# Performance work log

Hardware: AMD Instinct MI355X
Metric: run time of the kernel (lower is better)

The kernel has to match this reference:

```python
import jax, jax.numpy as jnp
import numpy as np

N = 30000      # nodes
E = 480000     # edges
F = 128        # num_node_features (== C, required by LSTM-JK stacking of h_list incl. x)
C = 128        # graph_hidden_channels
K = 8          # kernel_size (num gaussians)
D = 2          # pseudo-coordinate dim
L = 4          # nlayers
H = (L * C) // 2   # PyG JK-LSTM hidden size = 256
NHID = 512
NOUT = 256
B = 1024       # number of graphs in batch
EPS = 1e-15


def setup_inputs() -> dict:
    key = jax.random.key(0)
    ks = jax.random.split(key, 24)
    s = 0.05
    inp = {}
    inp['x'] = jax.random.normal(ks[0], (N, F), jnp.float32)
    inp['edge_index'] = jax.random.randint(ks[1], (2, E), 0, N, dtype=jnp.int32)
    inp['edge_attr'] = jax.random.uniform(ks[2], (E, D), jnp.float32)
    inp['batch'] = jnp.sort(jax.random.randint(ks[3], (N,), 0, B, dtype=jnp.int32))
    # GMMConv params per layer (Cin == C for all layers since F == C)
    inp['g'] = jax.random.normal(ks[4], (L, F, K * C), jnp.float32) * s
    inp['root'] = jax.random.normal(ks[5], (L, F, C), jnp.float32) * s
    inp['bias'] = jnp.zeros((L, C), jnp.float32)
    inp['mu'] = jax.random.uniform(ks[6], (L, K, D), jnp.float32)
    inp['sigma'] = jax.random.uniform(ks[7], (L, K, D), jnp.float32) * 0.5 + 0.5
    inp['bn_gamma'] = jnp.ones((L, C), jnp.float32)
    inp['bn_beta'] = jnp.zeros((L, C), jnp.float32)
    # Bidirectional LSTM for JumpingKnowledge: dir 0 = fwd, dir 1 = bwd; gate order i,f,g,o
    inp['w_ih'] = jax.random.normal(ks[8], (2, 4 * H, C), jnp.float32) * s
    inp['w_hh'] = jax.random.normal(ks[9], (2, 4 * H, H), jnp.float32) * s
    inp['b_ih'] = jnp.zeros((2, 4 * H), jnp.float32)
    inp['b_hh'] = jnp.zeros((2, 4 * H), jnp.float32)
    inp['att_w'] = jax.random.normal(ks[10], (2 * H, 1), jnp.float32) * s
    inp['att_b'] = jnp.zeros((1,), jnp.float32)
    inp['p1_w'] = jax.random.normal(ks[11], (C, NHID), jnp.float32) * s
    inp['p1_b'] = jnp.zeros((NHID,), jnp.float32)
    inp['p2_w'] = jax.random.normal(ks[12], (NHID, NOUT), jnp.float32) * s
    inp['p2_b'] = jnp.zeros((NOUT,), jnp.float32)
    inp['ln_g'] = jnp.ones((NOUT,), jnp.float32)
    inp['ln_b'] = jnp.zeros((NOUT,), jnp.float32)
    return inp


def _lstm_dir(xs, w_ih, w_hh, b_ih, b_hh, reverse):
    # xs: [T, N, C] -> hidden states [T, N, H], aligned with input order
    def step(carry, xt):
        h, c = carry
        gates = xt @ w_ih.T + h @ w_hh.T + (b_ih + b_hh)
        i, f, g, o = jnp.split(gates, 4, axis=-1)
        c = jax.nn.sigmoid(f) * c + jax.nn.sigmoid(i) * jnp.tanh(g)
        h = jax.nn.sigmoid(o) * jnp.tanh(c)
        return (h, c), h
    h0 = jnp.zeros((xs.shape[1], w_hh.shape[1]), xs.dtype)
    _, hs = jax.lax.scan(step, (h0, h0), xs, reverse=reverse)
    return hs


def reference(x, edge_index, edge_attr, batch, g, root, bias, mu, sigma,
              bn_gamma, bn_beta, w_ih, w_hh, b_ih, b_hh, att_w, att_b,
              p1_w, p1_b, p2_w, p2_b, ln_g, ln_b):
    src, dst = edge_index[0], edge_index[1]
    deg = jnp.maximum(jax.ops.segment_sum(jnp.ones((E,), x.dtype), dst, num_segments=N), 1.0)[:, None]
    h = x
    h_list = [x]
    for i in range(L):
        # GMMConv: node-level transform then gaussian-weighted message passing (mean aggr)
        xg = (h @ g[i]).reshape(N, K, C)                     # [N, K, C]
        diff = edge_attr[:, None, :] - mu[i][None]           # [E, K, D]
        w = jnp.exp(jnp.sum(-0.5 * diff ** 2 / (EPS + sigma[i][None] ** 2), axis=-1))  # [E, K]
        msg = jnp.zeros((E, C), x.dtype)
        for k in range(K):                                   # small fixed K; avoids [E,K,C] gather
            msg = msg + w[:, k:k + 1] * xg[src, k, :]
        agg = jax.ops.segment_sum(msg, dst, num_segments=N) / deg
        h = agg + h @ root[i] + bias[i]
        # BatchNorm1d (training-mode batch statistics)
        mean = h.mean(0)
        var = h.var(0)
        h = (h - mean) / jnp.sqrt(var + 1e-5) * bn_gamma[i] + bn_beta[i]
        if i < L - 1:
            h = jax.nn.relu(h)
        # dropout is identity in eval mode
        h_list.append(h)
    # JumpingKnowledge, mode='lstm'
    xs = jnp.stack(h_list, axis=0)                           # [L+1, N, C]
    hf = _lstm_dir(xs, w_ih[0], w_hh[0], b_ih[0], b_hh[0], False)
    hb = _lstm_dir(xs, w_ih[1], w_hh[1], b_ih[1], b_hh[1], True)
    seq = jnp.concatenate([hf, hb], axis=-1)                 # [L+1, N, 2H]
    alpha = (seq @ att_w)[..., 0] + att_b[0]                 # [L+1, N]
    alpha = jax.nn.softmax(alpha, axis=0)
    node_rep = jnp.sum(alpha[..., None] * xs, axis=0)        # [N, C]
    # global_mean_pool
    cnt = jnp.maximum(jax.ops.segment_sum(jnp.ones((N,), x.dtype), batch, num_segments=B), 1.0)
    h_graph = jax.ops.segment_sum(node_rep, batch, num_segments=B) / cnt[:, None]
    z = jax.nn.relu(h_graph @ p1_w + p1_b)
    z = z @ p2_w + p2_b
    zm = z.mean(-1, keepdims=True)
    zv = z.var(-1, keepdims=True)
    return (z - zm) / jnp.sqrt(zv + 1e-5) * ln_g + ln_b
```

## Files before the change

kernel.cpp:

```cpp
#include <hip/hip_runtime.h>
#include <hip/hip_bf16.h>
#include <math.h>

#define N_    30000
#define E_    480000
#define C_    128
#define K_    8
#define L_    4
#define H_    256
#define NHID_ 512
#define NOUT_ 256
#define B_    1024
#define SCAN_B 30

typedef __attribute__((ext_vector_type(8))) short short8;
typedef __attribute__((ext_vector_type(4))) float floatx4;
typedef __hip_bfloat16 bf16;

static inline size_t align256(size_t x){ return (x + 255) & ~(size_t)255; }

__device__ __forceinline__ void gload_lds16(const void* g, void* l){
  __builtin_amdgcn_global_load_lds((const __attribute__((address_space(1))) void*)g,
                                   (__attribute__((address_space(3))) void*)l, 16, 0, 0);
}
__device__ __forceinline__ float sigm_f(float x){ return __builtin_amdgcn_rcpf(1.f + __expf(-x)); }
__device__ __forceinline__ float tanh_f(float x){ return 1.f - 2.f*__builtin_amdgcn_rcpf(1.f + __expf(2.f*x)); }

__global__ void hist_k(const int* __restrict__ dst, int* __restrict__ cnt){
  int e = blockIdx.x*256 + threadIdx.x;
  if (e < E_) atomicAdd(&cnt[dst[e]], 1);
}

__global__ void scan1_k(const int* __restrict__ cnt, int* __restrict__ rowptr, int* __restrict__ btot){
  __shared__ int sh[1024];
  int i = blockIdx.x*1024 + (int)threadIdx.x;
  int v = (i < N_) ? cnt[i] : 0;
  sh[threadIdx.x] = v;
  __syncthreads();
  for (int o = 1; o < 1024; o <<= 1){
    int t = (threadIdx.x >= (unsigned)o) ? sh[threadIdx.x - o] : 0;
    __syncthreads();
    sh[threadIdx.x] += t;
    __syncthreads();
  }
  if (i < N_) rowptr[i] = sh[threadIdx.x] - v;
  if (threadIdx.x == 1023) btot[blockIdx.x] = sh[1023];
}
__global__ void scan2_k(const int* __restrict__ btot, int* __restrict__ boff){
  if (threadIdx.x == 0){
    int s = 0;
    for (int b = 0; b < SCAN_B; b++){ boff[b] = s; s += btot[b]; }
    boff[SCAN_B] = s;
  }
}
__global__ void scan3_k(int* __restrict__ rowptr, const int* __restrict__ boff){
  int i = blockIdx.x*1024 + (int)threadIdx.x;
  if (i < N_) rowptr[i] += boff[blockIdx.x];
  if (i == N_-1) rowptr[N_] = boff[SCAN_B];
}

__global__ void degf_k(const int* __restrict__ cnt, float* __restrict__ degf){
  int n = blockIdx.x*256 + threadIdx.x;
  if (n < N_) degf[n] = fmaxf((float)cnt[n], 1.0f);
}

__global__ void scatter_k(const int* __restrict__ src, const int* __restrict__ dst,
                          const int* __restrict__ rowptr, int* __restrict__ fill,
                          int* __restrict__ srcsort, int* __restrict__ edgepos){
  int e = blockIdx.x*256 + threadIdx.x;
  if (e >= E_) return;
  int d = dst[e];
  int pos = rowptr[d] + atomicAdd(&fill[d], 1);
  srcsort[pos] = src[e];
  edgepos[e] = pos;
}

__global__ void cast_k(const float* __restrict__ in, bf16* __restrict__ out, int n){
  int i = blockIdx.x*256 + threadIdx.x;
  if (i < n) out[i] = __float2bfloat16(in[i]);
}
__global__ void tcast_k(const float* __restrict__ in, bf16* __restrict__ out, int R, int Cc){
  const float* ip = in + (size_t)blockIdx.y*R*Cc;
  bf16* op = out + (size_t)blockIdx.y*R*Cc;
  int i = blockIdx.x*256 + threadIdx.x;
  if (i >= R*Cc) return;
  int c = i / R, r = i - c*R;
  op[i] = __float2bfloat16(ip[(size_t)r*Cc + c]);
}
__global__ void gtcast_k(const float* __restrict__ in, bf16* __restrict__ out){
  const float* ip = in + (size_t)blockIdx.y*C_*(K_*C_);
  bf16* op = out + (size_t)blockIdx.y*C_*(K_*C_);
  int i = blockIdx.x*256 + threadIdx.x;
  int co = i >> 10;
  int rem = i & 1023;
  int k = rem >> 7, c = rem & 127;
  op[i] = __float2bfloat16(ip[(size_t)c*(K_*C_) + k*C_ + co]);
}
__global__ void permcast_k(const float* __restrict__ in, bf16* __restrict__ out, int Kdim){
  const float* ip = in + (size_t)blockIdx.y*1024*Kdim;
  bf16* op = out + (size_t)blockIdx.y*1024*Kdim;
  int i = blockIdx.x*256 + threadIdx.x;
  if (i >= 1024*Kdim) return;
  int r = i / Kdim, k = i - r*Kdim;
  int gsel = r >> 8, jj = r & 255;
  int p = ((jj >> 5) << 7) + (((jj >> 4) & 1) << 6) + (gsel << 4) + (jj & 15);
  op[(size_t)p*Kdim + k] = __float2bfloat16(ip[i]);
}
__global__ void biassum_k(const float* __restrict__ bih, const float* __restrict__ bhh,
                          float* __restrict__ bs){
  int i = blockIdx.x*256 + threadIdx.x;
  if (i < 2048) bs[i] = bih[i] + bhh[i];
}

template<int OUTBF16, int STATS>
__global__ __launch_bounds__(256)
void gemm_bf16_k(const bf16* __restrict__ A1, const bf16* __restrict__ B1, int K1,
                 const bf16* __restrict__ A2, const bf16* __restrict__ B2, int K2,
                 const float* __restrict__ bias1, const float* __restrict__ bias2,
                 void* __restrict__ Cout, int M, int Nn, int relu,
                 float* __restrict__ stats)
{
  __shared__ short As[128*32];
  __shared__ short Bs[128*32];
  __shared__ float colstat[256];
  const int tid  = threadIdx.x;
  const int wave = tid >> 6, lane = tid & 63;
  const int m0 = blockIdx.y*128, n0 = blockIdx.x*128;
  const int wm = (wave >> 1)*64, wn = (wave & 1)*64;
  const int lrow = lane & 15, lk = lane >> 4;
  floatx4 acc[4][4] = {};
  if (STATS) colstat[tid] = 0.f;

  #pragma unroll
  for (int phase = 0; phase < 2; ++phase){
    const bf16* A = phase ? A2 : A1;
    const bf16* B = phase ? B2 : B1;
    const int   K = phase ? K2 : K1;
    if (A == nullptr) continue;
    for (int k0 = 0; k0 < K; k0 += 32){
      #pragma unroll
      for (int i = 0; i < 2; ++i){
        const int chunkbase = i*256 + wave*64;
        const int c   = chunkbase + lane;
        const int row = c >> 2, cc = (c & 3) << 3;
        int ar = m0 + row; if (ar >= M) ar = M - 1;
        gload_lds16(A + (size_t)ar*K + k0 + cc,        As + (size_t)chunkbase*8);
        gload_lds16(B + (size_t)(n0 + row)*K + k0 + cc, Bs + (size_t)chunkbase*8);
      }
      __syncthreads();
      short8 af[4], bfr[4];
      #pragma unroll
      for (int t = 0; t < 4; ++t){
        af[t]  = *(const short8*)&As[((size_t)(wm + t*16 + lrow))*32 + lk*8];
        bfr[t] = *(const short8*)&Bs[((size_t)(wn + t*16 + lrow))*32 + lk*8];
      }
      #pragma unroll
      for (int mt = 0; mt < 4; ++mt)
        #pragma unroll
        for (int nt = 0; nt < 4; ++nt)
          acc[mt][nt] = __builtin_amdgcn_mfma_f32_16x16x32_bf16(af[mt], bfr[nt], acc[mt][nt], 0, 0, 0);
      __syncthreads();
    }
  }

  float* outf = (float*)Cout;
  bf16*  outb = (bf16*)Cout;
  #pragma unroll
  for (int nt = 0; nt < 4; ++nt){
    const int col = n0 + wn + nt*16 + lrow;
    float bv = bias1 ? bias1[col] : 0.f;
    if (bias2) bv += bias2[col];
    float s = 0.f, s2 = 0.f;
    #pragma unroll
    for (int mt = 0; mt < 4; ++mt){
      #pragma unroll
      for (int r = 0; r < 4; ++r){
        const int row = m0 + wm + mt*16 + lk*4 + r;
        if (row >= M) continue;
        float v = acc[mt][nt][r] + bv;
        if (relu) v = fmaxf(v, 0.f);
        if (OUTBF16) outb[(size_t)row*Nn + col] = __float2bfloat16(v);
        else         outf[(size_t)row*Nn + col] = v;
        if (STATS){ s += v; s2 += v*v; }
      }
    }
    if (STATS){
      s  += __shfl_down(s, 16);  s  += __shfl_down(s, 32);
      s2 += __shfl_down(s2, 16); s2 += __shfl_down(s2, 32);
      if (lane < 16){
        atomicAdd(&colstat[wn + nt*16 + lane], s);
        atomicAdd(&colstat[128 + wn + nt*16 + lane], s2);
      }
    }
  }
  if (STATS){
    __syncthreads();
    if (tid < 128){
      atomicAdd(&stats[tid],       colstat[tid]);
      atomicAdd(&stats[128 + tid], colstat[128 + tid]);
    }
  }
}

__global__ __launch_bounds__(256)
void lstm_step_k(const bf16* __restrict__ A1, const bf16* __restrict__ B1,
                 const bf16* __restrict__ A2, const bf16* __restrict__ B2,
                 const float* __restrict__ bsum,
                 bf16* __restrict__ hout, bf16* __restrict__ cst,
                 const float* __restrict__ attw, float* __restrict__ alpha,
                 int M)
{
  __shared__ short As[128*32];
  __shared__ short Bs[128*32];
  const int tid  = threadIdx.x;
  const int wave = tid >> 6, lane = tid & 63;
  const int m0 = blockIdx.y*128, n0 = blockIdx.x*128;
  const int wm = (wave >> 1)*64, wn = (wave & 1)*64;
  const int lrow = lane & 15, lk = lane >> 4;
  floatx4 acc[4][4] = {};

  #pragma unroll
  for (int phase = 0; phase < 2; ++phase){
    const bf16* A = phase ? A2 : A1;
    const bf16* B = phase ? B2 : B1;
    const int   K = phase ? H_ : C_;
    if (A == nullptr) continue;
    for (int k0 = 0; k0 < K; k0 += 32){
      #pragma unroll
      for (int i = 0; i < 2; ++i){
        const int chunkbase = i*256 + wave*64;
        const int c   = chunkbase + lane;
        const int row = c >> 2, cc = (c & 3) << 3;
        int ar = m0 + row; if (ar >= M) ar = M - 1;
        gload_lds16(A + (size_t)ar*K + k0 + cc,        As + (size_t)chunkbase*8);
        gload_lds16(B + (size_t)(n0 + row)*K + k0 + cc, Bs + (size_t)chunkbase*8);
      }
      __syncthreads();
      short8 af[4], bfr[4];
      #pragma unroll
      for (int t = 0; t < 4; ++t){
        af[t]  = *(const short8*)&As[((size_t)(wm + t*16 + lrow))*32 + lk*8];
        bfr[t] = *(const short8*)&Bs[((size_t)(wn + t*16 + lrow))*32 + lk*8];
      }
      #pragma unroll
      for (int mt = 0; mt < 4; ++mt)
        #pragma unroll
        for (int nt = 0; nt < 4; ++nt)
          acc[mt][nt] = __builtin_amdgcn_mfma_f32_16x16x32_bf16(af[mt], bfr[nt], acc[mt][nt], 0, 0, 0);
      __syncthreads();
    }
  }

  const int j  = blockIdx.x*32 + (wave & 1)*16 + lrow;
  const float bi = bsum[0*H_ + j], bff = bsum[1*H_ + j];
  const float bg = bsum[2*H_ + j], bo  = bsum[3*H_ + j];
  const float aw = attw[j];
  #pragma unroll
  for (int mt = 0; mt < 4; ++mt){
    #pragma unroll
    for (int r = 0; r < 4; ++r){
      const int row = m0 + wm + mt*16 + lk*4 + r;
      const bool ok = row < M;
      const size_t idx = (size_t)row*H_ + j;
      float co = 0.f;
      if (A2 && ok) co = __bfloat162float(cst[idx]);
      float ig = sigm_f(acc[mt][0][r] + bi);
      float fg = sigm_f(acc[mt][1][r] + bff);
      float gt = tanh_f(acc[mt][2][r] + bg);
      float og = sigm_f(acc[mt][3][r] + bo);
      float cv = fg*co + ig*gt;
      float hv = og*tanh_f(cv);
      if (ok){
        cst[idx]  = __float2bfloat16(cv);
        hout[idx] = __float2bfloat16(hv);
      }
      float att = ok ? hv*aw : 0.f;
      att += __shfl_xor(att, 1);
      att += __shfl_xor(att, 2);
      att += __shfl_xor(att, 4);
      att += __shfl_xor(att, 8);
      if (lrow == 0 && ok) atomicAdd(&alpha[row], att);
    }
  }
}

__global__ void compute_w_k(const float* __restrict__ ea, const float* __restrict__ mu,
                            const float* __restrict__ sigma, const int* __restrict__ edgepos,
                            float* __restrict__ wsrt)
{
  int e = blockIdx.x*256 + threadIdx.x;
  if (e >= E_) return;
  float a0 = ea[2*e], a1 = ea[2*e+1];
  int pos = edgepos[e];
  float outv[8];
  #pragma unroll
  for (int k = 0; k < 8; k++){
    float d0 = a0 - mu[2*k],   d1 = a1 - mu[2*k+1];
    float s0 = sigma[2*k],     s1 = sigma[2*k+1];
    float t = -0.5f*(d0*d0/(1e-15f + s0*s0) + d1*d1/(1e-15f + s1*s1));
    outv[k] = expf(t);
  }
  float4* op = (float4*)(wsrt + (size_t)pos*8);
  op[0] = make_float4(outv[0], outv[1], outv[2], outv[3]);
  op[1] = make_float4(outv[4], outv[5], outv[6], outv[7]);
}

__global__ __launch_bounds__(256)
void aggregate_t_k(const bf16* __restrict__ h, const float* __restrict__ wsrt,
                   const int* __restrict__ rowptr, const int* __restrict__ srcsort,
                   const float* __restrict__ degf, bf16* __restrict__ t)
{
  int node = blockIdx.x*4 + (threadIdx.x >> 6);
  int lane = threadIdx.x & 63;
  if (node >= N_) return;
  int p0 = rowptr[node], p1 = rowptr[node+1];
  float ax[8] = {}, ay[8] = {};
  for (int p = p0; p < p1; p++){
    int s = srcsort[p];
    const float4 w03 = *(const float4*)(wsrt + (size_t)p*8);
    const float4 w47 = *(const float4*)(wsrt + (size_t)p*8 + 4);
    const float wk[8] = {w03.x,w03.y,w03.z,w03.w,w47.x,w47.y,w47.z,w47.w};
    float2 v = __bfloat1622float2(((const __hip_bfloat162*)(h + (size_t)s*C_))[lane]);
    #pragma unroll
    for (int k = 0; k < 8; k++){
      ax[k] = fmaf(wk[k], v.x, ax[k]);
      ay[k] = fmaf(wk[k], v.y, ay[k]);
    }
  }
  float inv = 1.0f / degf[node];
  __hip_bfloat162* tp = (__hip_bfloat162*)(t + (size_t)node*(K_*C_));
  #pragma unroll
  for (int k = 0; k < 8; k++){
    __hip_bfloat162 o; o.x = __float2bfloat16(ax[k]*inv); o.y = __float2bfloat16(ay[k]*inv);
    tp[k*64 + lane] = o;
  }
}

__global__ void bn_apply_k(const float* __restrict__ hpre, const float* __restrict__ stats,
                           const float* __restrict__ gamma, const float* __restrict__ beta,
                           bf16* __restrict__ outp, int relu)
{
  int i = blockIdx.x*256 + threadIdx.x;
  if (i >= N_*C_) return;
  int c = i & 127;
  float mean = stats[c] * (1.0f/N_);
  float var  = stats[c+128] * (1.0f/N_) - mean*mean;
  float rstd = rsqrtf(var + 1e-5f);
  float v = (hpre[i] - mean)*rstd*gamma[c] + beta[c];
  if (relu) v = fmaxf(v, 0.f);
  outp[i] = __float2bfloat16(v);
}

__global__ void jk_pool_k(const float* __restrict__ x, const bf16* __restrict__ hlist,
                          const float* __restrict__ alpha, const int* __restrict__ batch,
                          float* __restrict__ hgraph, float* __restrict__ gcnt)
{
  int n = blockIdx.x, c = threadIdx.x;
  float a[5]; float mx = -1e30f;
  #pragma unroll
  for (int t = 0; t < 5; t++){ a[t] = alpha[(size_t)t*N_ + n]; mx = fmaxf(mx, a[t]); }
  float ssum = 0.f;
  #pragma unroll
  for (int t = 0; t < 5; t++){ a[t] = expf(a[t] - mx); ssum += a[t]; }
  float inv = 1.0f/ssum;
  float val = a[0]*inv*x[(size_t)n*C_ + c];
  #pragma unroll
  for (int t = 1; t < 5; t++)
    val = fmaf(a[t]*inv, __bfloat162float(hlist[((size_t)(t-1)*N_ + n)*C_ + c]), val);
  int bg = batch[n];
  atomicAdd(&hgraph[(size_t)bg*C_ + c], val);
  if (c == 0) atomicAdd(&gcnt[bg], 1.0f);
}

__global__ void pool_div_k(const float* __restrict__ hg, const float* __restrict__ gcnt,
                           bf16* __restrict__ hgb){
  int i = blockIdx.x*256 + threadIdx.x;
  if (i < B_*C_) hgb[i] = __float2bfloat16(hg[i] / fmaxf(gcnt[i >> 7], 1.0f));
}

__global__ __launch_bounds__(256)
void layernorm_k(float* __restrict__ z, const float* __restrict__ g, const float* __restrict__ b){
  int row = blockIdx.x, j = threadIdx.x;
  float v = z[(size_t)row*NOUT_ + j];
  float s = v, s2 = v*v;
  #pragma unroll
  for (int o = 32; o; o >>= 1){ s += __shfl_down(s, o); s2 += __shfl_down(s2, o); }
  __shared__ float sh[8];
  int w = j >> 6;
  if ((j & 63) == 0){ sh[w] = s; sh[4+w] = s2; }
  __syncthreads();
  float st  = sh[0] + sh[1] + sh[2] + sh[3];
  float st2 = sh[4] + sh[5] + sh[6] + sh[7];
  float mean = st * (1.0f/NOUT_);
  float var  = st2 * (1.0f/NOUT_) - mean*mean;
  float rstd = rsqrtf(var + 1e-5f);
  z[(size_t)row*NOUT_ + j] = (v - mean)*rstd*g[j] + b[j];
}

extern "C" void kernel_launch(void* const* d_in, const int* in_sizes, int n_in,
                              void* d_out, int out_size, void* d_ws, size_t ws_size,
                              hipStream_t stream)
{
  (void)in_sizes; (void)n_in; (void)out_size; (void)ws_size;
  const float* x     = (const float*)d_in[0];
  const int*   eidx  = (const int*)  d_in[1];
  const float* eattr = (const float*)d_in[2];
  const int*   batch = (const int*)  d_in[3];
  const float* g     = (const float*)d_in[4];
  const float* root  = (const float*)d_in[5];
  const float* bias  = (const float*)d_in[6];
  const float* mu    = (const float*)d_in[7];
  const float* sigma = (const float*)d_in[8];
  const float* bng   = (const float*)d_in[9];
  const float* bnb   = (const float*)d_in[10];
  const float* w_ih  = (const float*)d_in[11];
  const float* w_hh  = (const float*)d_in[12];
  const float* b_ih  = (const float*)d_in[13];
  const float* b_hh  = (const float*)d_in[14];
  const float* attw  = (const float*)d_in[15];
  const float* p1w   = (const float*)d_in[17];
  const float* p1b   = (const float*)d_in[18];
  const float* p2w   = (const float*)d_in[19];
  const float* p2b   = (const float*)d_in[20];
  const float* lng   = (const float*)d_in[21];
  const float* lnb   = (const float*)d_in[22];
  float* outp = (float*)d_out;

  const int* src = eidx;
  const int* dst = eidx + E_;

  size_t off = 0;
  char* wsb = (char*)d_ws;
  auto carve = [&](size_t bytes)->void*{ void* p = wsb + off; off = align256(off + bytes); return p; };
  bf16*  hlist  = (bf16*) carve((size_t)L_*N_*C_*2);
  void*  big    =         carve((size_t)N_*(K_*C_)*2);
  void*  uni    =         carve((size_t)3*N_*H_*2 + 256);
  bf16*  xb     = (bf16*) carve((size_t)N_*C_*2);
  float* alpha  = (float*)carve((size_t)(L_+1)*N_*4);
  float* hgraph = (float*)carve((size_t)B_*C_*4);
  bf16*  hgb    = (bf16*) carve((size_t)B_*C_*2);
  float* gcnt   = (float*)carve((size_t)B_*4);
  bf16*  z1b    = (bf16*) carve((size_t)B_*NHID_*2);
  float* bnstats= (float*)carve((size_t)L_*2*C_*4);
  float* degf   = (float*)carve((size_t)N_*4);
  int* cnt      = (int*)  carve((size_t)N_*4);
  int* rowptr   = (int*)  carve((size_t)(N_+1)*4);
  int* fill     = (int*)  carve((size_t)N_*4);
  int* srcsort  = (int*)  carve((size_t)E_*4);
  int* edgepos  = (int*)  carve((size_t)E_*4);
  int* btot     = (int*)  carve((size_t)(SCAN_B+1)*4);
  int* boff     = (int*)  carve((size_t)(SCAN_B+1)*4);
  bf16* gGT   = (bf16*)carve((size_t)L_*C_*(K_*C_)*2);
  bf16* rootT = (bf16*)carve((size_t)L_*C_*C_*2);
  bf16* wihp  = (bf16*)carve((size_t)2*4*H_*C_*2);
  bf16* whhp  = (bf16*)carve((size_t)2*4*H_*H_*2);
  float* bsum = (float*)carve((size_t)2*4*H_*4);
  bf16* p1T   = (bf16*)carve((size_t)NHID_*C_*2);
  bf16* p2T   = (bf16*)carve((size_t)NOUT_*NHID_*2);

  float* wsrt   = (float*)uni;
  float* hpre   = wsrt + (size_t)E_*K_;
  bf16*  hA     = (bf16*)uni;
  bf16*  hB     = hA + (size_t)N_*H_;
  bf16*  cstate = hB + (size_t)N_*H_;
  bf16*  tbuf   = (bf16*)big;

  hipMemsetAsync(cnt,     0, (size_t)N_*4, stream);
  hipMemsetAsync(fill,    0, (size_t)N_*4, stream);
  hipMemsetAsync(bnstats, 0, (size_t)L_*2*C_*4, stream);
  hipMemsetAsync(hgraph,  0, (size_t)B_*C_*4, stream);
  hipMemsetAsync(gcnt,    0, (size_t)B_*4, stream);
  hipMemsetAsync(alpha,   0, (size_t)(L_+1)*N_*4, stream);

  const dim3 blk(256);

  hist_k  <<<(E_+255)/256, 256, 0, stream>>>(dst, cnt);
  scan1_k <<<SCAN_B, 1024, 0, stream>>>(cnt, rowptr, btot);
  scan2_k <<<1, 64, 0, stream>>>(btot, boff);
  scan3_k <<<SCAN_B, 1024, 0, stream>>>(rowptr, boff);
  degf_k  <<<(N_+255)/256, 256, 0, stream>>>(cnt, degf);
  scatter_k<<<(E_+255)/256, 256, 0, stream>>>(src, dst, rowptr, fill, srcsort, edgepos);

  cast_k <<<(N_*C_+255)/256, blk, 0, stream>>>(x, xb, N_*C_);
  gtcast_k<<<dim3((C_*K_*C_)/256, L_), blk, 0, stream>>>(g, gGT);
  tcast_k<<<dim3((C_*C_+255)/256,   L_), blk, 0, stream>>>(root, rootT, C_,   C_);
  permcast_k<<<dim3((1024*C_+255)/256, 2), blk, 0, stream>>>(w_ih, wihp, C_);
  permcast_k<<<dim3((1024*H_+255)/256, 2), blk, 0, stream>>>(w_hh, whhp, H_);
  biassum_k<<<8, blk, 0, stream>>>(b_ih, b_hh, bsum);
  tcast_k<<<dim3((C_*NHID_+255)/256, 1), blk, 0, stream>>>(p1w, p1T, C_,    NHID_);
  tcast_k<<<dim3((NHID_*NOUT_+255)/256,1), blk, 0, stream>>>(p2w, p2T, NHID_, NOUT_);

  const int MB = (N_ + 127)/128;

  for (int l = 0; l < L_; l++){
    const bf16* hin = l ? (hlist + (size_t)(l-1)*N_*C_) : xb;
    compute_w_k<<<(E_+255)/256, blk, 0, stream>>>(eattr, mu + (size_t)l*K_*2, sigma + (size_t)l*K_*2, edgepos, wsrt);
    aggregate_t_k<<<N_/4, blk, 0, stream>>>(hin, wsrt, rowptr, srcsort, degf, tbuf);
    gemm_bf16_k<0,1><<<dim3(C_/128, MB), blk, 0, stream>>>(
        tbuf, gGT + (size_t)l*C_*K_*C_, K_*C_, hin, rootT + (size_t)l*C_*C_, C_,
        bias + (size_t)l*C_, nullptr, hpre, N_, C_, 0, bnstats + l*2*C_);
    bn_apply_k<<<(N_*C_+255)/256, blk, 0, stream>>>(hpre, bnstats + l*2*C_, bng + (size_t)l*C_, bnb + (size_t)l*C_,
                                                    hlist + (size_t)l*N_*C_, (l < L_-1) ? 1 : 0);
  }

  for (int dir = 0; dir < 2; dir++){
    const bf16* wih = wihp + (size_t)dir*4*H_*C_;
    const bf16* whh = whhp + (size_t)dir*4*H_*H_;
    const float* bsd = bsum + (size_t)dir*4*H_;
    const bf16* hprev = nullptr;
    for (int s = 0; s < 5; s++){
      int t = dir ? 4 - s : s;
      const bf16* xt = t ? (hlist + (size_t)(t-1)*N_*C_) : xb;
      bf16* hnext = (s & 1) ? hB : hA;
      lstm_step_k<<<dim3(8, MB), blk, 0, stream>>>(
          xt, wih, hprev, whh, bsd, hnext, cstate,
          attw + (size_t)dir*H_, alpha + (size_t)t*N_, N_);
      hprev = hnext;
    }
  }

  jk_pool_k<<<N_, 128, 0, stream>>>(x, hlist, alpha, batch, hgraph, gcnt);
  pool_div_k<<<(B_*C_+255)/256, blk, 0, stream>>>(hgraph, gcnt, hgb);

  gemm_bf16_k<1,0><<<dim3(NHID_/128, B_/128), blk, 0, stream>>>(
      hgb, p1T, C_, nullptr, nullptr, 0, p1b, nullptr, z1b, B_, NHID_, 1, nullptr);
  gemm_bf16_k<0,0><<<dim3(NOUT_/128, B_/128), blk, 0, stream>>>(
      z1b, p2T, NHID_, nullptr, nullptr, 0, p2b, nullptr, outp, B_, NOUT_, 0, nullptr);
  layernorm_k<<<B_, 256, 0, stream>>>(outp, lng, lnb);
}
```

Baseline: 1.324 ms.

## Batch both LSTM directions per launch and store sorted edge weights in bf16

The forward and backward LSTM recurrences now run in a single launch per step, with blockIdx.z selecting the direction. This halves the number of LSTM launches and doubles the grid size, so more of the GPU is occupied per step. Edge attributes are also permuted into dst-sorted order once in scatter_k, so compute_w_k writes coalesced bf16 Gaussian weights rather than scattered fp32 ones. The aggregation then reads half as many weight bytes. In exchange, the weights lose precision (bf16 instead of fp32) and the workspace needs twice as much LSTM state buffer space.

```diff
diff --git a/kernel.cpp b/kernel.cpp
--- a/kernel.cpp
+++ b/kernel.cpp
@@ -22,6 +22,9 @@
 __device__ __forceinline__ void gload_lds16(const void* g, void* l){
   __builtin_amdgcn_global_load_lds((const __attribute__((address_space(1))) void*)g,
                                    (__attribute__((address_space(3))) void*)l, 16, 0, 0);
+}
+__device__ __forceinline__ float bf2f(short s){
+  union { unsigned u; float f; } x; x.u = ((unsigned)(unsigned short)s) << 16; return x.f;
 }
 __device__ __forceinline__ float sigm_f(float x){ return __builtin_amdgcn_rcpf(1.f + __expf(-x)); }
 __device__ __forceinline__ float tanh_f(float x){ return 1.f - 2.f*__builtin_amdgcn_rcpf(1.f + __expf(2.f*x)); }
@@ -65,14 +68,15 @@
 }
 
 __global__ void scatter_k(const int* __restrict__ src, const int* __restrict__ dst,
+                          const float* __restrict__ ea,
                           const int* __restrict__ rowptr, int* __restrict__ fill,
-                          int* __restrict__ srcsort, int* __restrict__ edgepos){
+                          int* __restrict__ srcsort, float* __restrict__ easort){
   int e = blockIdx.x*256 + threadIdx.x;
   if (e >= E_) return;
   int d = dst[e];
   int pos = rowptr[d] + atomicAdd(&fill[d], 1);
   srcsort[pos] = src[e];
-  edgepos[e] = pos;
+  ((float2*)easort)[pos] = ((const float2*)ea)[e];
 }
 
 __global__ void cast_k(const float* __restrict__ in, bf16* __restrict__ out, int n){
@@ -203,15 +207,29 @@
 }
 
 __global__ __launch_bounds__(256)
-void lstm_step_k(const bf16* __restrict__ A1, const bf16* __restrict__ B1,
-                 const bf16* __restrict__ A2, const bf16* __restrict__ B2,
-                 const float* __restrict__ bsum,
-                 bf16* __restrict__ hout, bf16* __restrict__ cst,
-                 const float* __restrict__ attw, float* __restrict__ alpha,
-                 int M)
+void lstm_step2_k(const bf16* __restrict__ A1f, const bf16* __restrict__ A1b,
+                  const bf16* __restrict__ wihp, const bf16* __restrict__ whhp,
+                  const bf16* __restrict__ hpf, const bf16* __restrict__ hpb,
+                  const float* __restrict__ bsum,
+                  bf16* __restrict__ hof, bf16* __restrict__ hob,
+                  bf16* __restrict__ csf, bf16* __restrict__ csb,
+                  const float* __restrict__ attw,
+                  float* __restrict__ alf, float* __restrict__ alb,
+                  int M)
 {
   __shared__ short As[128*32];
   __shared__ short Bs[128*32];
+  const int dir = blockIdx.z;
+  const bf16* A1 = dir ? A1b : A1f;
+  const bf16* A2 = dir ? hpb : hpf;
+  const bf16* B1 = wihp + (size_t)dir*4*H_*C_;
+  const bf16* B2 = whhp + (size_t)dir*4*H_*H_;
+  bf16* hout = dir ? hob : hof;
+  bf16* cst  = dir ? csb : csf;
+  float* alpha = dir ? alb : alf;
+  const float* bsd = bsum + (size_t)dir*4*H_;
+  const float* awd = attw + (size_t)dir*H_;
+
   const int tid  = threadIdx.x;
   const int wave = tid >> 6, lane = tid & 63;
   const int m0 = blockIdx.y*128, n0 = blockIdx.x*128;
@@ -252,9 +270,9 @@
   }
 
   const int j  = blockIdx.x*32 + (wave & 1)*16 + lrow;
-  const float bi = bsum[0*H_ + j], bff = bsum[1*H_ + j];
-  const float bg = bsum[2*H_ + j], bo  = bsum[3*H_ + j];
-  const float aw = attw[j];
+  const float bi = bsd[0*H_ + j], bff = bsd[1*H_ + j];
+  const float bg = bsd[2*H_ + j], bo  = bsd[3*H_ + j];
+  const float aw = awd[j];
   #pragma unroll
   for (int mt = 0; mt < 4; ++mt){
     #pragma unroll
@@ -284,29 +302,25 @@
   }
 }
 
-__global__ void compute_w_k(const float* __restrict__ ea, const float* __restrict__ mu,
-                            const float* __restrict__ sigma, const int* __restrict__ edgepos,
-                            float* __restrict__ wsrt)
+__global__ void compute_w_k(const float* __restrict__ easort, const float* __restrict__ mu,
+                            const float* __restrict__ sigma, bf16* __restrict__ wsrt)
 {
   int e = blockIdx.x*256 + threadIdx.x;
   if (e >= E_) return;
-  float a0 = ea[2*e], a1 = ea[2*e+1];
-  int pos = edgepos[e];
-  float outv[8];
+  float2 a = ((const float2*)easort)[e];
+  short8 o;
   #pragma unroll
   for (int k = 0; k < 8; k++){
-    float d0 = a0 - mu[2*k],   d1 = a1 - mu[2*k+1];
+    float d0 = a.x - mu[2*k],  d1 = a.y - mu[2*k+1];
     float s0 = sigma[2*k],     s1 = sigma[2*k+1];
     float t = -0.5f*(d0*d0/(1e-15f + s0*s0) + d1*d1/(1e-15f + s1*s1));
-    outv[k] = expf(t);
-  }
-  float4* op = (float4*)(wsrt + (size_t)pos*8);
-  op[0] = make_float4(outv[0], outv[1], outv[2], outv[3]);
-  op[1] = make_float4(outv[4], outv[5], outv[6], outv[7]);
+    o[k] = __builtin_bit_cast(short, __float2bfloat16(expf(t)));
+  }
+  *(short8*)(wsrt + (size_t)e*8) = o;
 }
 
 __global__ __launch_bounds__(256)
-void aggregate_t_k(const bf16* __restrict__ h, const float* __restrict__ wsrt,
+void aggregate_t_k(const bf16* __restrict__ h, const bf16* __restrict__ wsrt,
                    const int* __restrict__ rowptr, const int* __restrict__ srcsort,
                    const float* __restrict__ degf, bf16* __restrict__ t)
 {
@@ -317,14 +331,13 @@
   float ax[8] = {}, ay[8] = {};
   for (int p = p0; p < p1; p++){
     int s = srcsort[p];
-    const float4 w03 = *(const float4*)(wsrt + (size_t)p*8);
-    const float4 w47 = *(const float4*)(wsrt + (size_t)p*8 + 4);
-    const float wk[8] = {w03.x,w03.y,w03.z,w03.w,w47.x,w47.y,w47.z,w47.w};
+    short8 wv = *(const short8*)(wsrt + (size_t)p*8);
     float2 v = __bfloat1622float2(((const __hip_bfloat162*)(h + (size_t)s*C_))[lane]);
     #pragma unroll
     for (int k = 0; k < 8; k++){
-      ax[k] = fmaf(wk[k], v.x, ax[k]);
-      ay[k] = fmaf(wk[k], v.y, ay[k]);
+      float wk = bf2f(wv[k]);
+      ax[k] = fmaf(wk, v.x, ax[k]);
+      ay[k] = fmaf(wk, v.y, ay[k]);
     }
   }
   float inv = 1.0f / degf[node];
@@ -434,7 +447,7 @@
   auto carve = [&](size_t bytes)->void*{ void* p = wsb + off; off = align256(off + bytes); return p; };
   bf16*  hlist  = (bf16*) carve((size_t)L_*N_*C_*2);
   void*  big    =         carve((size_t)N_*(K_*C_)*2);
-  void*  uni    =         carve((size_t)3*N_*H_*2 + 256);
+  void*  uni    =         carve((size_t)6*N_*H_*2 + 256);
   bf16*  xb     = (bf16*) carve((size_t)N_*C_*2);
   float* alpha  = (float*)carve((size_t)(L_+1)*N_*4);
   float* hgraph = (float*)carve((size_t)B_*C_*4);
@@ -447,7 +460,7 @@
   int* rowptr   = (int*)  carve((size_t)(N_+1)*4);
   int* fill     = (int*)  carve((size_t)N_*4);
   int* srcsort  = (int*)  carve((size_t)E_*4);
-  int* edgepos  = (int*)  carve((size_t)E_*4);
+  float* easort = (float*)carve((size_t)E_*2*4);
   int* btot     = (int*)  carve((size_t)(SCAN_B+1)*4);
   int* boff     = (int*)  carve((size_t)(SCAN_B+1)*4);
   bf16* gGT   = (bf16*)carve((size_t)L_*C_*(K_*C_)*2);
@@ -458,11 +471,14 @@
   bf16* p1T   = (bf16*)carve((size_t)NHID_*C_*2);
   bf16* p2T   = (bf16*)carve((size_t)NOUT_*NHID_*2);
 
-  float* wsrt   = (float*)uni;
-  float* hpre   = wsrt + (size_t)E_*K_;
-  bf16*  hA     = (bf16*)uni;
-  bf16*  hB     = hA + (size_t)N_*H_;
-  bf16*  cstate = hB + (size_t)N_*H_;
+  bf16*  wsrt   = (bf16*)uni;
+  float* hpre   = (float*)((char*)uni + (size_t)E_*K_*2);
+  bf16*  hAf    = (bf16*)uni;
+  bf16*  hAb    = hAf + (size_t)N_*H_;
+  bf16*  hBf    = hAb + (size_t)N_*H_;
+  bf16*  hBb    = hBf + (size_t)N_*H_;
+  bf16*  csf    = hBb + (size_t)N_*H_;
+  bf16*  csb    = csf + (size_t)N_*H_;
   bf16*  tbuf   = (bf16*)big;
 
   hipMemsetAsync(cnt,     0, (size_t)N_*4, stream);
@@ -479,7 +495,7 @@
   scan2_k <<<1, 64, 0, stream>>>(btot, boff);
   scan3_k <<<SCAN_B, 1024, 0, stream>>>(rowptr, boff);
   degf_k  <<<(N_+255)/256, 256, 0, stream>>>(cnt, degf);
-  scatter_k<<<(E_+255)/256, 256, 0, stream>>>(src, dst, rowptr, fill, srcsort, edgepos);
+  scatter_k<<<(E_+255)/256, 256, 0, stream>>>(src, dst, eattr, rowptr, fill, srcsort, easort);
 
   cast_k <<<(N_*C_+255)/256, blk, 0, stream>>>(x, xb, N_*C_);
   gtcast_k<<<dim3((C_*K_*C_)/256, L_), blk, 0, stream>>>(g, gGT);
@@ -494,7 +510,7 @@
 
   for (int l = 0; l < L_; l++){
     const bf16* hin = l ? (hlist + (size_t)(l-1)*N_*C_) : xb;
-    compute_w_k<<<(E_+255)/256, blk, 0, stream>>>(eattr, mu + (size_t)l*K_*2, sigma + (size_t)l*K_*2, edgepos, wsrt);
+    compute_w_k<<<(E_+255)/256, blk, 0, stream>>>(easort, mu + (size_t)l*K_*2, sigma + (size_t)l*K_*2, wsrt);
     aggregate_t_k<<<N_/4, blk, 0, stream>>>(hin, wsrt, rowptr, srcsort, degf, tbuf);
     gemm_bf16_k<0,1><<<dim3(C_/128, MB), blk, 0, stream>>>(
         tbuf, gGT + (size_t)l*C_*K_*C_, K_*C_, hin, rootT + (size_t)l*C_*C_, C_,
@@ -503,19 +519,18 @@
                                                     hlist + (size_t)l*N_*C_, (l < L_-1) ? 1 : 0);
   }
 
-  for (int dir = 0; dir < 2; dir++){
-    const bf16* wih = wihp + (size_t)dir*4*H_*C_;
-    const bf16* whh = whhp + (size_t)dir*4*H_*H_;
-    const float* bsd = bsum + (size_t)dir*4*H_;
-    const bf16* hprev = nullptr;
+  {
+    const bf16 *hpf = nullptr, *hpb = nullptr;
     for (int s = 0; s < 5; s++){
-      int t = dir ? 4 - s : s;
-      const bf16* xt = t ? (hlist + (size_t)(t-1)*N_*C_) : xb;
-      bf16* hnext = (s & 1) ? hB : hA;
-      lstm_step_k<<<dim3(8, MB), blk, 0, stream>>>(
-          xt, wih, hprev, whh, bsd, hnext, cstate,
-          attw + (size_t)dir*H_, alpha + (size_t)t*N_, N_);
-      hprev = hnext;
+      int tf = s, tb = 4 - s;
+      const bf16* xtf = tf ? (hlist + (size_t)(tf-1)*N_*C_) : xb;
+      const bf16* xtb = tb ? (hlist + (size_t)(tb-1)*N_*C_) : xb;
+      bf16* hof = (s & 1) ? hBf : hAf;
+      bf16* hob = (s & 1) ? hBb : hAb;
+      lstm_step2_k<<<dim3(8, MB, 2), blk, 0, stream>>>(
+          xtf, xtb, wihp, whhp, hpf, hpb, bsum, hof, hob, csf, csb,
+          attw, alpha + (size_t)tf*N_, alpha + (size_t)tb*N_, N_);
+      hpf = hof; hpb = hob;
     }
   }
 
```

New measurement: 1.256 ms. 1.05x faster.
